# Performance work log

Measured on AMD Instinct MI355X. Metric: run time of the kernel, lower is better.

The kernel has to match this reference:

```python
import jax, jax.numpy as jnp
import numpy as np

NUM_USERS = 100000
NUM_ITEMS = 50000
NUM_EDGES = 4000000
EMB_DIM = 64
K_HOPS = 3


def setup_inputs() -> dict:
    key = jax.random.key(0)
    k1, k2, k3, k4, k5, k6 = jax.random.split(key, 6)
    N = NUM_USERS + NUM_ITEMS
    return {
        "users_emb": jax.random.normal(k1, (NUM_USERS, EMB_DIM), dtype=jnp.float32) * 0.1,
        "items_emb": jax.random.normal(k2, (NUM_ITEMS, EMB_DIM), dtype=jnp.float32) * 0.1,
        "edge_row": jax.random.randint(k3, (NUM_EDGES,), 0, N, dtype=jnp.int32),
        "edge_col": jax.random.randint(k4, (NUM_EDGES,), 0, N, dtype=jnp.int32),
        "user_id": jax.random.randint(k5, (4096,), 0, NUM_USERS, dtype=jnp.int32),
        "item_ids": jax.random.randint(k6, (4096,), 0, NUM_ITEMS, dtype=jnp.int32),
    }


def reference(users_emb, items_emb, edge_row, edge_col, user_id, item_ids):
    num_users = users_emb.shape[0]
    N = num_users + items_emb.shape[0]
    dt = users_emb.dtype

    # gcn_norm (no self loops): deg = rowsum of A, w_e = d_r^{-1/2} d_c^{-1/2}
    deg = jax.ops.segment_sum(jnp.ones(edge_row.shape[0], dtype=dt), edge_row,
                              num_segments=N)
    deg_inv_sqrt = jnp.where(deg > 0, 1.0 / jnp.sqrt(jnp.where(deg > 0, deg, 1.0)), 0.0)
    w = deg_inv_sqrt[edge_row] * deg_inv_sqrt[edge_col]  # [E]

    emb = jnp.concatenate([users_emb, items_emb], axis=0)  # [N, D]
    acc = emb  # running sum of K+1 layer snapshots
    for _ in range(K_HOPS):
        # SpMM: out[r] += w_e * emb[c]
        emb = jax.ops.segment_sum(w[:, None] * emb[edge_col], edge_row,
                                  num_segments=N)
        acc = acc + emb
    emb_final = acc / (K_HOPS + 1)  # layer-mean pooling

    users_final = emb_final[user_id]               # [B, D]
    items_final = emb_final[num_users + item_ids]  # [B, D]
    return jnp.concatenate([users_final, items_final], axis=1)  # [B, 2D]
```

## Files before the change

kernel.cpp:

```cpp
#include <hip/hip_runtime.h>
#include <hip/hip_bf16.h>

#define NUSERS 100000
#define NITEMS 50000
#define NN (NUSERS + NITEMS)
#define NE 4000000
#define DIM 64
#define BQ 4096
#define NBIN ((NN + 255) >> 8)
#define BINCAP 9216
#define EPB2 8192

typedef unsigned short u16;
typedef unsigned int u32;
typedef float v2f __attribute__((ext_vector_type(2)));
typedef unsigned u32x2 __attribute__((ext_vector_type(2)));

__device__ __forceinline__ float bf2f(u16 u) {
    return __uint_as_float(((unsigned)u) << 16);
}
__device__ __forceinline__ u16 f2bf(float f) {
    unsigned x = __float_as_uint(f);
    return (u16)((x + 0x7FFFu + ((x >> 16) & 1u)) >> 16);
}
__device__ __forceinline__ void add8p(v2f* acc2, uint4 u) {
    acc2[0] += (v2f){__uint_as_float(u.x << 16), __uint_as_float(u.x & 0xffff0000u)};
    acc2[1] += (v2f){__uint_as_float(u.y << 16), __uint_as_float(u.y & 0xffff0000u)};
    acc2[2] += (v2f){__uint_as_float(u.z << 16), __uint_as_float(u.z & 0xffff0000u)};
    acc2[3] += (v2f){__uint_as_float(u.w << 16), __uint_as_float(u.w & 0xffff0000u)};
}
__device__ __forceinline__ uint4 ld_row(const char* __restrict__ base, int c, int dgoff) {
    u32 off = ((u32)c << 7) + (u32)dgoff;
    return *(const uint4*)(base + off);
}

#if __has_builtin(__builtin_amdgcn_update_dpp)
__device__ __forceinline__ float xadd8(float x) {
    int y = __builtin_amdgcn_update_dpp(0, __float_as_int(x), 0x128, 0xF, 0xF, true);
    return x + __int_as_float(y);
}
#else
__device__ __forceinline__ float xadd8(float x) { return x + __shfl_xor(x, 8, 64); }
#endif
#if __has_builtin(__builtin_amdgcn_permlane16_swap)
__device__ __forceinline__ float xadd16(float x) {
    u32x2 r = __builtin_amdgcn_permlane16_swap(__float_as_uint(x), __float_as_uint(x),
                                               false, false);
    return __uint_as_float(r.x) + __uint_as_float(r.y);
}
#else
__device__ __forceinline__ float xadd16(float x) { return x + __shfl_xor(x, 16, 64); }
#endif
#if __has_builtin(__builtin_amdgcn_permlane32_swap)
__device__ __forceinline__ float xadd32(float x) {
    u32x2 r = __builtin_amdgcn_permlane32_swap(__float_as_uint(x), __float_as_uint(x),
                                               false, false);
    return __uint_as_float(r.x) + __uint_as_float(r.y);
}
#else
__device__ __forceinline__ float xadd32(float x) { return x + __shfl_xor(x, 32, 64); }
#endif

__device__ __forceinline__ void reduce_acc(v2f* acc2) {
#pragma unroll
    for (int j = 0; j < 4; ++j) { acc2[j].x = xadd8(acc2[j].x);  acc2[j].y = xadd8(acc2[j].y);  }
#pragma unroll
    for (int j = 0; j < 4; ++j) { acc2[j].x = xadd16(acc2[j].x); acc2[j].y = xadd16(acc2[j].y); }
#pragma unroll
    for (int j = 0; j < 4; ++j) { acc2[j].x = xadd32(acc2[j].x); acc2[j].y = xadd32(acc2[j].y); }
}

template<int G>
__device__ __forceinline__ void rowsum_fix(const int* __restrict__ col_s, int start,
                                           int eslot, const char* __restrict__ inb,
                                           int dgoff, v2f* acc2) {
    int cg[G];
#pragma unroll
    for (int g = 0; g < G; ++g) cg[g] = col_s[start + (g << 3) + eslot];
    uint4 v[G];
#pragma unroll
    for (int g = 0; g < G; ++g) v[g] = ld_row(inb, cg[g], dgoff);
#if __has_builtin(__builtin_amdgcn_sched_barrier)
    __builtin_amdgcn_sched_barrier(0);
#endif
#pragma unroll
    for (int g = 0; g < G; ++g) add8p(acc2, v[g]);
}

__device__ __forceinline__ void rowsum_core(int start, int n8,
                                            const int* __restrict__ col_s,
                                            const char* __restrict__ inb,
                                            int eslot, int dgoff, v2f* acc2) {
    switch (n8 >> 3) {
    case 0: break;
    case 1: rowsum_fix<1>(col_s, start, eslot, inb, dgoff, acc2); break;
    case 2: rowsum_fix<2>(col_s, start, eslot, inb, dgoff, acc2); break;
    case 3: rowsum_fix<3>(col_s, start, eslot, inb, dgoff, acc2); break;
    case 4: rowsum_fix<4>(col_s, start, eslot, inb, dgoff, acc2); break;
    case 5: rowsum_fix<5>(col_s, start, eslot, inb, dgoff, acc2); break;
    case 6: rowsum_fix<6>(col_s, start, eslot, inb, dgoff, acc2); break;
    case 7: rowsum_fix<7>(col_s, start, eslot, inb, dgoff, acc2); break;
    case 8: rowsum_fix<8>(col_s, start, eslot, inb, dgoff, acc2); break;
    default: {
        int i = eslot;
        int c0 = col_s[start + i];
        uint4 v0 = ld_row(inb, c0, dgoff);
        for (i += 8; i < n8; i += 8) {
            int c1 = col_s[start + i];
            uint4 v1 = ld_row(inb, c1, dgoff);
            add8p(acc2, v0);
            v0 = v1;
        }
        add8p(acc2, v0);
    }
    }
}

__global__ void k_init(int* __restrict__ bin_cur, u32* __restrict__ m2w,
                       u16* __restrict__ ea, u16* __restrict__ eb) {
    int t = blockIdx.x * blockDim.x + threadIdx.x;
    if (t < NBIN) bin_cur[t] = t * BINCAP;
    if (t < 37504) m2w[t] = 0;
    if (t < 32) {
        ((u32*)(ea + (size_t)NN * DIM))[t] = 0;
        ((u32*)(eb + (size_t)NN * DIM))[t] = 0;
    }
}

__global__ void __launch_bounds__(1024) k_binA2(
        const int* __restrict__ row, const int* __restrict__ col,
        int* __restrict__ bin_cur, u32* __restrict__ pairs, int E) {
    __shared__ u32 stage[EPB2];
    __shared__ int hist[NBIN];
    __shared__ int base_l[NBIN];
    __shared__ int cbase[NBIN];
    __shared__ int lcur[NBIN];
    __shared__ int s[1024];
    int t = threadIdx.x;
    int base = blockIdx.x * EPB2;
    int lim = min(E - base, EPB2);

    if (t < NBIN) hist[t] = 0;
    __syncthreads();

    for (int i = t; i < lim; i += 1024)
        atomicAdd(&hist[row[base + i] >> 8], 1);
    __syncthreads();

    int v = (t < NBIN) ? hist[t] : 0;
    s[t] = v;
    __syncthreads();
    for (int off = 1; off < 1024; off <<= 1) {
        int x = (t >= off) ? s[t - off] : 0;
        __syncthreads();
        s[t] += x;
        __syncthreads();
    }
    if (t < NBIN) {
        int excl = s[t] - v;
        base_l[t] = excl;
        lcur[t] = excl;
        cbase[t] = (v > 0) ? atomicAdd(&bin_cur[t], v) : 0;
    }
    __syncthreads();

    for (int i = t; i < lim; i += 1024) {
        int r = row[base + i];
        int c = col[base + i];
        int pos = atomicAdd(&lcur[r >> 8], 1);
        stage[pos] = ((u32)(r & 255) << 24) | (u32)c;
    }
    __syncthreads();

    int wv = t >> 6;
    int lane = t & 63;
    for (int b = wv; b < NBIN; b += 16) {
        int h = hist[b];
        int lb = base_l[b];
        size_t gb = (size_t)cbase[b];
        for (int i = lane; i < h; i += 64)
            pairs[gb + i] = stage[lb + i];
    }
}

__global__ void __launch_bounds__(1024) k_binB(
        const u32* __restrict__ pairs, const int* __restrict__ bin_cur,
        int* __restrict__ col_s, int* __restrict__ rs, int* __restrict__ deg) {
    __shared__ int cnt[256];
    __shared__ int pscan[256];
    __shared__ int cur[256];
    int b = blockIdx.x;
    int t = threadIdx.x;
    int base = b * BINCAP;
    int end = bin_cur[b];
    if (t < 256) cnt[t] = 0;
    __syncthreads();
    for (int i = base + t; i < end; i += 1024)
        atomicAdd(&cnt[pairs[i] >> 24], 1);
    __syncthreads();
    int v = (t < 256) ? cnt[t] : 0;
    int pv = (v + 7) & ~7;
    if (t < 256) pscan[t] = pv;
    __syncthreads();
    for (int off = 1; off < 256; off <<= 1) {
        int x = (t >= off && t < 256) ? pscan[t - off] : 0;
        __syncthreads();
        if (t < 256) pscan[t] += x;
        __syncthreads();
    }
    if (t < 256) {
        int rowstart = base + pscan[t] - pv;
        int r = (b << 8) + t;
        if (r < NN) {
            rs[r] = rowstart;
            deg[r] = v;
        }
        cur[t] = rowstart;
        for (int i = v; i < pv; ++i) col_s[rowstart + i] = NN;
    }
    __syncthreads();
    for (int i = base + t; i < end; i += 1024) {
        u32 p = pairs[i];
        int pos = atomicAdd(&cur[p >> 24], 1);
        col_s[pos] = (int)(p & 0x00FFFFFFu);
    }
}

__global__ void k_concat_t0(const float* __restrict__ u, const float* __restrict__ it,
                            const int* __restrict__ deg, u16* __restrict__ emb) {
    int i = blockIdx.x * blockDim.x + threadIdx.x;
    const int NU4 = NUSERS * DIM / 4;
    const int NT4 = NN * DIM / 4;
    if (i >= NT4) return;
    int row = i >> 4;
    int d = deg[row];
    float sc = (d > 0) ? (1.0f / sqrtf((float)d)) : 0.0f;
    float4 v = (i < NU4) ? ((const float4*)u)[i] : ((const float4*)it)[i - NU4];
    ushort4 o;
    o.x = f2bf(sc * v.x); o.y = f2bf(sc * v.y);
    o.z = f2bf(sc * v.z); o.w = f2bf(sc * v.w);
    ((ushort4*)emb)[i] = o;
}

__global__ void k_mark(const int* __restrict__ uid, const int* __restrict__ iid,
                       const int* __restrict__ rs, const int* __restrict__ deg,
                       const int* __restrict__ col_s, unsigned char* __restrict__ m2) {
    int q = (blockIdx.x * blockDim.x + threadIdx.x) >> 6;
    if (q >= 2 * BQ) return;
    int lane = threadIdx.x & 63;
    int r = (q < BQ) ? uid[q] : (NUSERS + iid[q - BQ]);
    if (lane == 0) m2[r] = 1;
    int s = rs[r], n = deg[r];
    for (int i = lane; i < n; i += 64) m2[col_s[s + i]] = 1;
}

__global__ void __launch_bounds__(256) k_spmm8(
        const int* __restrict__ rs, const int* __restrict__ deg,
        const int* __restrict__ col_s, const u16* __restrict__ in,
        u16* __restrict__ out, const unsigned char* __restrict__ mask) {
    int wid = (blockIdx.x * blockDim.x + threadIdx.x) >> 6;
    if (wid >= NN) return;
    if (mask && !mask[wid]) return;
    int lane = threadIdx.x & 63;
    int eslot = lane >> 3;
    int dg = lane & 7;
    int dgoff = dg << 4;
    int n = deg[wid];
    int start = rs[wid];
    int n8 = (n + 7) & ~7;
    const char* inb = (const char*)in;
    v2f acc2[4] = {(v2f)0.f, (v2f)0.f, (v2f)0.f, (v2f)0.f};
    if (n8 > 0)
        rowsum_core(start, n8, col_s, inb, eslot, dgoff, acc2);
    reduce_acc(acc2);
    if (eslot == 0) {
        float s = (n > 0) ? (1.0f / (float)n) : 0.0f;
        v2f vs = {s, s};
        u32 p[4];
#pragma unroll
        for (int j = 0; j < 4; ++j) {
            v2f r = acc2[j] * vs;
            __hip_bfloat162 h = __float22bfloat162_rn(make_float2(r.x, r.y));
            p[j] = *(u32*)&h;
        }
        ((uint4*)out)[(size_t)wid * 8 + dg] = make_uint4(p[0], p[1], p[2], p[3]);
    }
}

__global__ void __launch_bounds__(256) k_spmm_out(
        const int* __restrict__ rs, const int* __restrict__ deg,
        const int* __restrict__ col_s, const u16* __restrict__ in,
        const int* __restrict__ uid, const int* __restrict__ iid,
        float* __restrict__ out) {
    int q = (blockIdx.x * blockDim.x + threadIdx.x) >> 6;
    if (q >= 2 * BQ) return;
    int lane = threadIdx.x & 63;
    int eslot = lane >> 3;
    int dg = lane & 7;
    int dgoff = dg << 4;
    int b, r, off;
    if (q < BQ) { b = q; r = uid[q]; off = 0; }
    else { b = q - BQ; r = NUSERS + iid[q - BQ]; off = DIM; }
    int n = deg[r];
    int start = rs[r];
    int n8 = (n + 7) & ~7;
    const char* inb = (const char*)in;
    v2f acc2[4] = {(v2f)0.f, (v2f)0.f, (v2f)0.f, (v2f)0.f};
    if (n8 > 0)
        rowsum_core(start, n8, col_s, inb, eslot, dgoff, acc2);
    reduce_acc(acc2);
    if (eslot == 0) {
        float dr = (n > 0) ? (1.0f / sqrtf((float)n)) : 0.0f;
        float* o = out + (size_t)b * (2 * DIM) + off + dg * 8;
#pragma unroll
        for (int j = 0; j < 4; ++j) {
            o[2 * j]     = (o[2 * j]     + dr * acc2[j].x) * 0.25f;
            o[2 * j + 1] = (o[2 * j + 1] + dr * acc2[j].y) * 0.25f;
        }
    }
}


__global__ void k_gather_init(const int* __restrict__ uid, const int* __restrict__ iid,
                              const float* __restrict__ u, const float* __restrict__ it,
                              float* __restrict__ out) {
    int t = blockIdx.x * blockDim.x + threadIdx.x;
    if (t >= BQ * DIM) return;
    int b = t >> 6;
    int d = t & 63;
    out[b * (2 * DIM) + d]       = u[(size_t)uid[b] * DIM + d];
    out[b * (2 * DIM) + DIM + d] = it[(size_t)iid[b] * DIM + d];
}

__global__ void k_gather_add(const int* __restrict__ uid, const int* __restrict__ iid,
                             const int* __restrict__ deg, const u16* __restrict__ emb,
                             float* __restrict__ out) {
    int t = blockIdx.x * blockDim.x + threadIdx.x;
    if (t >= BQ * DIM) return;
    int b = t >> 6;
    int d = t & 63;
    int ru = uid[b];
    int ri = NUSERS + iid[b];
    int du = deg[ru], di = deg[ri];
    float su = (du > 0) ? sqrtf((float)du) : 0.0f;
    float si = (di > 0) ? sqrtf((float)di) : 0.0f;
    int ou = b * (2 * DIM) + d;
    int oi = ou + DIM;
    out[ou] = out[ou] + su * bf2f(emb[(size_t)ru * DIM + d]);
    out[oi] = out[oi] + si * bf2f(emb[(size_t)ri * DIM + d]);
}


extern "C" void kernel_launch(void* const* d_in, const int* in_sizes, int n_in,
                              void* d_out, int out_size, void* d_ws, size_t ws_size,
                              hipStream_t stream) {
    const float* users_emb = (const float*)d_in[0];
    const float* items_emb = (const float*)d_in[1];
    const int*   edge_row  = (const int*)d_in[2];
    const int*   edge_col  = (const int*)d_in[3];
    const int*   user_id   = (const int*)d_in[4];
    const int*   item_ids  = (const int*)d_in[5];
    float* out = (float*)d_out;

    char* ws = (char*)d_ws;
    int*   deg_i   = (int*)  (ws + 0);
    int*   rs      = (int*)  (ws + 655360);
    int*   bin_cur = (int*)  (ws + 1310720);
    unsigned char* m2 = (unsigned char*)(ws + 1400000);
    int*   col_s   = (int*)  (ws + 4194304);
    u32*   pairs   = (u32*)  (ws + 29360128);
    u16*   emb_a   = (u16*)  (ws + 54525952);
    u16*   emb_b   = (u16*)  (ws + 75497472);

    k_init<<<147, 256, 0, stream>>>(bin_cur, (u32*)m2, emb_a, emb_b);

    k_binA2<<<(NE + EPB2 - 1) / EPB2, 1024, 0, stream>>>(edge_row, edge_col, bin_cur,
                                                         pairs, NE);
    k_binB<<<NBIN, 1024, 0, stream>>>(pairs, bin_cur, col_s, rs, deg_i);

    k_concat_t0<<<(NN * DIM / 4 + 255) / 256, 256, 0, stream>>>(users_emb, items_emb,
                                                                deg_i, emb_a);

    k_gather_init<<<(BQ * DIM + 255) / 256, 256, 0, stream>>>(user_id, item_ids,
                                                              users_emb, items_emb, out);

    k_mark<<<(2 * BQ + 3) / 4, 256, 0, stream>>>(user_id, item_ids, rs, deg_i, col_s, m2);

    const int spmm_blocks = (NN + 3) / 4;
    k_spmm8<<<spmm_blocks, 256, 0, stream>>>(rs, deg_i, col_s, emb_a, emb_b,
                                             (const unsigned char*)nullptr);
    k_gather_add<<<(BQ * DIM + 255) / 256, 256, 0, stream>>>(user_id, item_ids, deg_i,
                                                             emb_b, out);
    k_spmm8<<<spmm_blocks, 256, 0, stream>>>(rs, deg_i, col_s, emb_b, emb_a, m2);
    k_gather_add<<<(BQ * DIM + 255) / 256, 256, 0, stream>>>(user_id, item_ids, deg_i,
                                                             emb_a, out);
    k_spmm_out<<<(2 * BQ + 3) / 4, 256, 0, stream>>>(rs, deg_i, col_s, emb_a,
                                                     user_id, item_ids, out);
}
```

Before: 307.7 us.

## Replace per-row SpMM with persistent software-pipelined kernel using packed row metadata

Replaces the one-wave-per-row SpMM with a persistent grid of 1024 blocks in which each wave strides over rows. The loop is software-pipelined: metadata for row i+3 is loaded, column indices for row i+2 are fetched, and embedding gathers for row i+1 are issued while row i is reduced and stored. Row start and degree are packed into an int2 array written by the binning kernel, so each row needs one metadata load. The aim is to hide gather latency and remove per-row launch and scheduling overhead, at the cost of many more live registers and lower occupancy; the masked pass also reads mask bytes for rows it will skip.

```diff
diff --git a/kernel.cpp b/kernel.cpp
--- a/kernel.cpp
+++ b/kernel.cpp
@@ -68,6 +68,113 @@
     for (int j = 0; j < 4; ++j) { acc2[j].x = xadd16(acc2[j].x); acc2[j].y = xadd16(acc2[j].y); }
 #pragma unroll
     for (int j = 0; j < 4; ++j) { acc2[j].x = xadd32(acc2[j].x); acc2[j].y = xadd32(acc2[j].y); }
+}
+
+struct MetaS { int s; int n; int m; };
+
+template<bool MASKED>
+__device__ __forceinline__ MetaS ldmeta(const int2* __restrict__ meta2,
+                                        const unsigned char* __restrict__ mask, int r) {
+    MetaS t; t.s = 0; t.n = 0; t.m = 0;
+    if (r < NN) {
+        int2 v = meta2[r];
+        t.s = v.x; t.n = v.y;
+        t.m = MASKED ? (int)mask[r] : 1;
+    }
+    return t;
+}
+
+__device__ __forceinline__ void ldcols(int* cg, const int* __restrict__ col_s,
+                                       MetaS mt, int eslot) {
+    int n8 = (mt.n + 7) & ~7;
+    int lim = mt.m ? n8 : 0;
+#pragma unroll
+    for (int g = 0; g < 8; ++g) {
+        int c = col_s[mt.s + (g << 3) + eslot];
+        cg[g] = ((g << 3) < lim) ? c : NN;
+    }
+}
+
+__device__ __forceinline__ void issue4(uint4* v, const char* __restrict__ base2,
+                                       const int* cg, int lo) {
+#pragma unroll
+    for (int g = 0; g < 4; ++g)
+        v[g] = *(const uint4*)(base2 + (((u32)cg[lo + g]) << 7));
+}
+
+__device__ __forceinline__ void consume_store(const uint4* v, int big, MetaS mt,
+        const int* __restrict__ col_s, const char* __restrict__ base2,
+        int eslot, int dg, u16* __restrict__ out, int r) {
+    v2f acc2[4] = {(v2f)0.f, (v2f)0.f, (v2f)0.f, (v2f)0.f};
+#pragma unroll
+    for (int g = 0; g < 4; ++g) add8p(acc2, v[g]);
+    if (big) {
+#pragma unroll
+        for (int g = 4; g < 8; ++g) add8p(acc2, v[g]);
+    }
+    int n8 = (mt.n + 7) & ~7;
+    if (n8 > 64) {
+        for (int i = 64 + eslot; i < n8; i += 8) {
+            int c = col_s[mt.s + i];
+            uint4 u = *(const uint4*)(base2 + (((u32)c) << 7));
+            add8p(acc2, u);
+        }
+    }
+    reduce_acc(acc2);
+    if (eslot == 0) {
+        float sc = (mt.n > 0) ? (1.0f / (float)mt.n) : 0.0f;
+        v2f vs = {sc, sc};
+        u32 p[4];
+#pragma unroll
+        for (int j = 0; j < 4; ++j) {
+            v2f t = acc2[j] * vs;
+            __hip_bfloat162 h = __float22bfloat162_rn(make_float2(t.x, t.y));
+            p[j] = *(u32*)&h;
+        }
+        ((uint4*)out)[(size_t)r * 8 + dg] = make_uint4(p[0], p[1], p[2], p[3]);
+    }
+}
+
+template<bool MASKED>
+__global__ void __launch_bounds__(256) k_spmm_p(
+        const int2* __restrict__ meta2, const int* __restrict__ col_s,
+        const u16* __restrict__ in, u16* __restrict__ out,
+        const unsigned char* __restrict__ mask) {
+    int lane = threadIdx.x & 63;
+    int eslot = lane >> 3, dg = lane & 7;
+    const char* base2 = (const char*)in + (dg << 4);
+    const int nw = gridDim.x << 2;
+    int r = ((blockIdx.x << 8) + threadIdx.x) >> 6;
+
+    MetaS M0 = ldmeta<MASKED>(meta2, mask, r);
+    MetaS M1 = ldmeta<MASKED>(meta2, mask, r + nw);
+    MetaS M2 = ldmeta<MASKED>(meta2, mask, r + 2 * nw);
+    int cgA[8], cgB[8];
+    uint4 vA[8], vB[8];
+    ldcols(cgA, col_s, M0, eslot);
+    int bigA = M0.m & (M0.n > 32), bigB = 0;
+    if (M0.m)  issue4(vA, base2, cgA, 0);
+    if (bigA)  issue4(vA + 4, base2, cgA, 4);
+    ldcols(cgB, col_s, M1, eslot);
+
+    for (;;) {
+        bigB = M1.m & (M1.n > 32);
+        if (M1.m) issue4(vB, base2, cgB, 0);
+        if (bigB) issue4(vB + 4, base2, cgB, 4);
+        ldcols(cgA, col_s, M2, eslot);
+        MetaS M3 = ldmeta<MASKED>(meta2, mask, r + 3 * nw);
+        if (M0.m) consume_store(vA, bigA, M0, col_s, base2, eslot, dg, out, r);
+        r += nw; if (r >= NN) break;
+        M0 = M1; M1 = M2; M2 = M3;
+        bigA = M1.m & (M1.n > 32);
+        if (M1.m) issue4(vA, base2, cgA, 0);
+        if (bigA) issue4(vA + 4, base2, cgA, 4);
+        ldcols(cgB, col_s, M2, eslot);
+        M3 = ldmeta<MASKED>(meta2, mask, r + 3 * nw);
+        if (M0.m) consume_store(vB, bigB, M0, col_s, base2, eslot, dg, out, r);
+        r += nw; if (r >= NN) break;
+        M0 = M1; M1 = M2; M2 = M3;
+    }
 }
 
 template<int G>
@@ -185,7 +292,8 @@
 
 __global__ void __launch_bounds__(1024) k_binB(
         const u32* __restrict__ pairs, const int* __restrict__ bin_cur,
-        int* __restrict__ col_s, int* __restrict__ rs, int* __restrict__ deg) {
+        int* __restrict__ col_s, int* __restrict__ rs, int* __restrict__ deg,
+        int2* __restrict__ meta2) {
     __shared__ int cnt[256];
     __shared__ int pscan[256];
     __shared__ int cur[256];
@@ -214,6 +322,7 @@
         if (r < NN) {
             rs[r] = rowstart;
             deg[r] = v;
+            meta2[r] = make_int2(rowstart, v);
         }
         cur[t] = rowstart;
         for (int i = v; i < pv; ++i) col_s[rowstart + i] = NN;
@@ -252,39 +361,6 @@
     if (lane == 0) m2[r] = 1;
     int s = rs[r], n = deg[r];
     for (int i = lane; i < n; i += 64) m2[col_s[s + i]] = 1;
-}
-
-__global__ void __launch_bounds__(256) k_spmm8(
-        const int* __restrict__ rs, const int* __restrict__ deg,
-        const int* __restrict__ col_s, const u16* __restrict__ in,
-        u16* __restrict__ out, const unsigned char* __restrict__ mask) {
-    int wid = (blockIdx.x * blockDim.x + threadIdx.x) >> 6;
-    if (wid >= NN) return;
-    if (mask && !mask[wid]) return;
-    int lane = threadIdx.x & 63;
-    int eslot = lane >> 3;
-    int dg = lane & 7;
-    int dgoff = dg << 4;
-    int n = deg[wid];
-    int start = rs[wid];
-    int n8 = (n + 7) & ~7;
-    const char* inb = (const char*)in;
-    v2f acc2[4] = {(v2f)0.f, (v2f)0.f, (v2f)0.f, (v2f)0.f};
-    if (n8 > 0)
-        rowsum_core(start, n8, col_s, inb, eslot, dgoff, acc2);
-    reduce_acc(acc2);
-    if (eslot == 0) {
-        float s = (n > 0) ? (1.0f / (float)n) : 0.0f;
-        v2f vs = {s, s};
-        u32 p[4];
-#pragma unroll
-        for (int j = 0; j < 4; ++j) {
-            v2f r = acc2[j] * vs;
-            __hip_bfloat162 h = __float22bfloat162_rn(make_float2(r.x, r.y));
-            p[j] = *(u32*)&h;
-        }
-        ((uint4*)out)[(size_t)wid * 8 + dg] = make_uint4(p[0], p[1], p[2], p[3]);
-    }
 }
 
 __global__ void __launch_bounds__(256) k_spmm_out(
@@ -367,6 +443,7 @@
     int*   rs      = (int*)  (ws + 655360);
     int*   bin_cur = (int*)  (ws + 1310720);
     unsigned char* m2 = (unsigned char*)(ws + 1400000);
+    int2*  meta2   = (int2*) (ws + 2097152);
     int*   col_s   = (int*)  (ws + 4194304);
     u32*   pairs   = (u32*)  (ws + 29360128);
     u16*   emb_a   = (u16*)  (ws + 54525952);
@@ -376,7 +453,7 @@
 
     k_binA2<<<(NE + EPB2 - 1) / EPB2, 1024, 0, stream>>>(edge_row, edge_col, bin_cur,
                                                          pairs, NE);
-    k_binB<<<NBIN, 1024, 0, stream>>>(pairs, bin_cur, col_s, rs, deg_i);
+    k_binB<<<NBIN, 1024, 0, stream>>>(pairs, bin_cur, col_s, rs, deg_i, meta2);
 
     k_concat_t0<<<(NN * DIM / 4 + 255) / 256, 256, 0, stream>>>(users_emb, items_emb,
                                                                 deg_i, emb_a);
@@ -386,12 +463,11 @@
 
     k_mark<<<(2 * BQ + 3) / 4, 256, 0, stream>>>(user_id, item_ids, rs, deg_i, col_s, m2);
 
-    const int spmm_blocks = (NN + 3) / 4;
-    k_spmm8<<<spmm_blocks, 256, 0, stream>>>(rs, deg_i, col_s, emb_a, emb_b,
-                                             (const unsigned char*)nullptr);
+    k_spmm_p<false><<<1024, 256, 0, stream>>>(meta2, col_s, emb_a, emb_b,
+                                              (const unsigned char*)nullptr);
     k_gather_add<<<(BQ * DIM + 255) / 256, 256, 0, stream>>>(user_id, item_ids, deg_i,
                                                              emb_b, out);
-    k_spmm8<<<spmm_blocks, 256, 0, stream>>>(rs, deg_i, col_s, emb_b, emb_a, m2);
+    k_spmm_p<true><<<1024, 256, 0, stream>>>(meta2, col_s, emb_b, emb_a, m2);
     k_gather_add<<<(BQ * DIM + 255) / 256, 256, 0, stream>>>(user_id, item_ids, deg_i,
                                                              emb_a, out);
     k_spmm_out<<<(2 * BQ + 3) / 4, 256, 0, stream>>>(rs, deg_i, col_s, emb_a,
```

New measurement: 341.9 us. 1.11x slower.

## Process two rows per wavefront in SpMM with packed row metadata

Applied to the files above, without the earlier changes.

Rewrites the SpMM kernels so each 64-lane wavefront handles two rows, 32 lanes each with 4 edge slots. The earlier design used one wave per row with 8 edge slots. Row start and degree are packed into one int2 array written by the binning kernel, so a single load replaces two. Edge loops become fixed batches of 8 loads with a wave-uniform tail loop instead of a degree switch. The aim is to cut idle lanes and reduction steps for the low average degree (~27), at the cost of divergence when paired rows have different degrees.

```diff
diff --git a/kernel.cpp b/kernel.cpp
--- a/kernel.cpp
+++ b/kernel.cpp
@@ -29,10 +29,6 @@
     acc2[2] += (v2f){__uint_as_float(u.z << 16), __uint_as_float(u.z & 0xffff0000u)};
     acc2[3] += (v2f){__uint_as_float(u.w << 16), __uint_as_float(u.w & 0xffff0000u)};
 }
-__device__ __forceinline__ uint4 ld_row(const char* __restrict__ base, int c, int dgoff) {
-    u32 off = ((u32)c << 7) + (u32)dgoff;
-    return *(const uint4*)(base + off);
-}
 
 #if __has_builtin(__builtin_amdgcn_update_dpp)
 __device__ __forceinline__ float xadd8(float x) {
@@ -51,68 +47,122 @@
 #else
 __device__ __forceinline__ float xadd16(float x) { return x + __shfl_xor(x, 16, 64); }
 #endif
-#if __has_builtin(__builtin_amdgcn_permlane32_swap)
-__device__ __forceinline__ float xadd32(float x) {
-    u32x2 r = __builtin_amdgcn_permlane32_swap(__float_as_uint(x), __float_as_uint(x),
-                                               false, false);
-    return __uint_as_float(r.x) + __uint_as_float(r.y);
-}
+
+#if __has_builtin(__builtin_amdgcn_sched_barrier)
+#define SCHED_FENCE() __builtin_amdgcn_sched_barrier(0)
 #else
-__device__ __forceinline__ float xadd32(float x) { return x + __shfl_xor(x, 32, 64); }
+#define SCHED_FENCE()
 #endif
 
-__device__ __forceinline__ void reduce_acc(v2f* acc2) {
+__device__ __forceinline__ void reduce_half(v2f* acc2) {
 #pragma unroll
     for (int j = 0; j < 4; ++j) { acc2[j].x = xadd8(acc2[j].x);  acc2[j].y = xadd8(acc2[j].y);  }
 #pragma unroll
     for (int j = 0; j < 4; ++j) { acc2[j].x = xadd16(acc2[j].x); acc2[j].y = xadd16(acc2[j].y); }
-#pragma unroll
-    for (int j = 0; j < 4; ++j) { acc2[j].x = xadd32(acc2[j].x); acc2[j].y = xadd32(acc2[j].y); }
-}
-
-template<int G>
-__device__ __forceinline__ void rowsum_fix(const int* __restrict__ col_s, int start,
-                                           int eslot, const char* __restrict__ inb,
-                                           int dgoff, v2f* acc2) {
-    int cg[G];
-#pragma unroll
-    for (int g = 0; g < G; ++g) cg[g] = col_s[start + (g << 3) + eslot];
-    uint4 v[G];
-#pragma unroll
-    for (int g = 0; g < G; ++g) v[g] = ld_row(inb, cg[g], dgoff);
-#if __has_builtin(__builtin_amdgcn_sched_barrier)
-    __builtin_amdgcn_sched_barrier(0);
-#endif
-#pragma unroll
-    for (int g = 0; g < G; ++g) add8p(acc2, v[g]);
-}
-
-__device__ __forceinline__ void rowsum_core(int start, int n8,
-                                            const int* __restrict__ col_s,
-                                            const char* __restrict__ inb,
-                                            int eslot, int dgoff, v2f* acc2) {
-    switch (n8 >> 3) {
-    case 0: break;
-    case 1: rowsum_fix<1>(col_s, start, eslot, inb, dgoff, acc2); break;
-    case 2: rowsum_fix<2>(col_s, start, eslot, inb, dgoff, acc2); break;
-    case 3: rowsum_fix<3>(col_s, start, eslot, inb, dgoff, acc2); break;
-    case 4: rowsum_fix<4>(col_s, start, eslot, inb, dgoff, acc2); break;
-    case 5: rowsum_fix<5>(col_s, start, eslot, inb, dgoff, acc2); break;
-    case 6: rowsum_fix<6>(col_s, start, eslot, inb, dgoff, acc2); break;
-    case 7: rowsum_fix<7>(col_s, start, eslot, inb, dgoff, acc2); break;
-    case 8: rowsum_fix<8>(col_s, start, eslot, inb, dgoff, acc2); break;
-    default: {
-        int i = eslot;
-        int c0 = col_s[start + i];
-        uint4 v0 = ld_row(inb, c0, dgoff);
-        for (i += 8; i < n8; i += 8) {
-            int c1 = col_s[start + i];
-            uint4 v1 = ld_row(inb, c1, dgoff);
-            add8p(acc2, v0);
-            v0 = v1;
-        }
-        add8p(acc2, v0);
-    }
+}
+
+__device__ __forceinline__ void batch8(const int* __restrict__ col_s, int start,
+                                       int s0, int lim, int eslot,
+                                       const char* __restrict__ base2, v2f* acc2) {
+    int cg[8];
+#pragma unroll
+    for (int g = 0; g < 8; ++g) {
+        int slot = s0 + (g << 2) + eslot;
+        int c = col_s[start + slot];
+        cg[g] = (slot < lim) ? c : NN;
+    }
+    uint4 v[8];
+#pragma unroll
+    for (int g = 0; g < 8; ++g)
+        v[g] = *(const uint4*)(base2 + (((u32)cg[g]) << 7));
+    SCHED_FENCE();
+#pragma unroll
+    for (int g = 0; g < 8; ++g) add8p(acc2, v[g]);
+}
+
+template<bool MASKED>
+__global__ void __launch_bounds__(256) k_spmm2(
+        const int2* __restrict__ meta2, const int* __restrict__ col_s,
+        const u16* __restrict__ in, u16* __restrict__ out,
+        const unsigned char* __restrict__ mask) {
+    int wid = (blockIdx.x * blockDim.x + threadIdx.x) >> 6;
+    int lane = threadIdx.x & 63;
+    int half = lane >> 5;
+    int eslot = (lane >> 3) & 3;
+    int dg = lane & 7;
+    int r = (wid << 1) + half;
+    int2 mv = meta2[r];
+    int start = mv.x, n = mv.y;
+    int m = MASKED ? (int)mask[r] : 1;
+    int n8 = (n + 7) & ~7;
+    int lim = m ? n8 : 0;
+    if (MASKED && !__any(lim > 0)) return;
+    const char* base2 = (const char*)in + (dg << 4);
+
+    v2f acc2[4] = {(v2f)0.f, (v2f)0.f, (v2f)0.f, (v2f)0.f};
+    batch8(col_s, start, 0, lim, eslot, base2, acc2);
+    if (__any(lim > 32))
+        batch8(col_s, start, 32, lim, eslot, base2, acc2);
+    if (__any(lim > 64)) {
+        for (int i = 64 + eslot; i < lim; i += 4) {
+            int c = col_s[start + i];
+            uint4 u = *(const uint4*)(base2 + (((u32)c) << 7));
+            add8p(acc2, u);
+        }
+    }
+    reduce_half(acc2);
+    if (eslot == 0 && m) {
+        float sc = (n > 0) ? (1.0f / (float)n) : 0.0f;
+        v2f vs = {sc, sc};
+        u32 p[4];
+#pragma unroll
+        for (int j = 0; j < 4; ++j) {
+            v2f t = acc2[j] * vs;
+            __hip_bfloat162 h = __float22bfloat162_rn(make_float2(t.x, t.y));
+            p[j] = *(u32*)&h;
+        }
+        ((uint4*)out)[(size_t)r * 8 + dg] = make_uint4(p[0], p[1], p[2], p[3]);
+    }
+}
+
+__global__ void __launch_bounds__(256) k_spmm_out2(
+        const int2* __restrict__ meta2, const int* __restrict__ col_s,
+        const u16* __restrict__ in, const int* __restrict__ uid,
+        const int* __restrict__ iid, float* __restrict__ out) {
+    int wid = (blockIdx.x * blockDim.x + threadIdx.x) >> 6;
+    int lane = threadIdx.x & 63;
+    int half = lane >> 5;
+    int eslot = (lane >> 3) & 3;
+    int dg = lane & 7;
+    int q = (wid << 1) + half;
+    int b, r, off;
+    if (q < BQ) { b = q; r = uid[q]; off = 0; }
+    else { b = q - BQ; r = NUSERS + iid[q - BQ]; off = DIM; }
+    int2 mv = meta2[r];
+    int start = mv.x, n = mv.y;
+    int n8 = (n + 7) & ~7;
+    const char* base2 = (const char*)in + (dg << 4);
+
+    v2f acc2[4] = {(v2f)0.f, (v2f)0.f, (v2f)0.f, (v2f)0.f};
+    batch8(col_s, start, 0, n8, eslot, base2, acc2);
+    if (__any(n8 > 32))
+        batch8(col_s, start, 32, n8, eslot, base2, acc2);
+    if (__any(n8 > 64)) {
+        for (int i = 64 + eslot; i < n8; i += 4) {
+            int c = col_s[start + i];
+            uint4 u = *(const uint4*)(base2 + (((u32)c) << 7));
+            add8p(acc2, u);
+        }
+    }
+    reduce_half(acc2);
+    if (eslot == 0) {
+        float dr = (n > 0) ? (1.0f / sqrtf((float)n)) : 0.0f;
+        float* o = out + (size_t)b * (2 * DIM) + off + dg * 8;
+#pragma unroll
+        for (int j = 0; j < 4; ++j) {
+            o[2 * j]     = (o[2 * j]     + dr * acc2[j].x) * 0.25f;
+            o[2 * j + 1] = (o[2 * j + 1] + dr * acc2[j].y) * 0.25f;
+        }
     }
 }
 
@@ -185,7 +235,8 @@
 
 __global__ void __launch_bounds__(1024) k_binB(
         const u32* __restrict__ pairs, const int* __restrict__ bin_cur,
-        int* __restrict__ col_s, int* __restrict__ rs, int* __restrict__ deg) {
+        int* __restrict__ col_s, int* __restrict__ rs, int* __restrict__ deg,
+        int2* __restrict__ meta2) {
     __shared__ int cnt[256];
     __shared__ int pscan[256];
     __shared__ int cur[256];
@@ -214,6 +265,7 @@
         if (r < NN) {
             rs[r] = rowstart;
             deg[r] = v;
+            meta2[r] = make_int2(rowstart, v);
         }
         cur[t] = rowstart;
         for (int i = v; i < pv; ++i) col_s[rowstart + i] = NN;
@@ -252,72 +304,6 @@
     if (lane == 0) m2[r] = 1;
     int s = rs[r], n = deg[r];
     for (int i = lane; i < n; i += 64) m2[col_s[s + i]] = 1;
-}
-
-__global__ void __launch_bounds__(256) k_spmm8(
-        const int* __restrict__ rs, const int* __restrict__ deg,
-        const int* __restrict__ col_s, const u16* __restrict__ in,
-        u16* __restrict__ out, const unsigned char* __restrict__ mask) {
-    int wid = (blockIdx.x * blockDim.x + threadIdx.x) >> 6;
-    if (wid >= NN) return;
-    if (mask && !mask[wid]) return;
-    int lane = threadIdx.x & 63;
-    int eslot = lane >> 3;
-    int dg = lane & 7;
-    int dgoff = dg << 4;
-    int n = deg[wid];
-    int start = rs[wid];
-    int n8 = (n + 7) & ~7;
-    const char* inb = (const char*)in;
-    v2f acc2[4] = {(v2f)0.f, (v2f)0.f, (v2f)0.f, (v2f)0.f};
-    if (n8 > 0)
-        rowsum_core(start, n8, col_s, inb, eslot, dgoff, acc2);
-    reduce_acc(acc2);
-    if (eslot == 0) {
-        float s = (n > 0) ? (1.0f / (float)n) : 0.0f;
-        v2f vs = {s, s};
-        u32 p[4];
-#pragma unroll
-        for (int j = 0; j < 4; ++j) {
-            v2f r = acc2[j] * vs;
-            __hip_bfloat162 h = __float22bfloat162_rn(make_float2(r.x, r.y));
-            p[j] = *(u32*)&h;
-        }
-        ((uint4*)out)[(size_t)wid * 8 + dg] = make_uint4(p[0], p[1], p[2], p[3]);
-    }
-}
-
-__global__ void __launch_bounds__(256) k_spmm_out(
-        const int* __restrict__ rs, const int* __restrict__ deg,
-        const int* __restrict__ col_s, const u16* __restrict__ in,
-        const int* __restrict__ uid, const int* __restrict__ iid,
-        float* __restrict__ out) {
-    int q = (blockIdx.x * blockDim.x + threadIdx.x) >> 6;
-    if (q >= 2 * BQ) return;
-    int lane = threadIdx.x & 63;
-    int eslot = lane >> 3;
-    int dg = lane & 7;
-    int dgoff = dg << 4;
-    int b, r, off;
-    if (q < BQ) { b = q; r = uid[q]; off = 0; }
-    else { b = q - BQ; r = NUSERS + iid[q - BQ]; off = DIM; }
-    int n = deg[r];
-    int start = rs[r];
-    int n8 = (n + 7) & ~7;
-    const char* inb = (const char*)in;
-    v2f acc2[4] = {(v2f)0.f, (v2f)0.f, (v2f)0.f, (v2f)0.f};
-    if (n8 > 0)
-        rowsum_core(start, n8, col_s, inb, eslot, dgoff, acc2);
-    reduce_acc(acc2);
-    if (eslot == 0) {
-        float dr = (n > 0) ? (1.0f / sqrtf((float)n)) : 0.0f;
-        float* o = out + (size_t)b * (2 * DIM) + off + dg * 8;
-#pragma unroll
-        for (int j = 0; j < 4; ++j) {
-            o[2 * j]     = (o[2 * j]     + dr * acc2[j].x) * 0.25f;
-            o[2 * j + 1] = (o[2 * j + 1] + dr * acc2[j].y) * 0.25f;
-        }
-    }
 }
 
 
@@ -367,6 +353,7 @@
     int*   rs      = (int*)  (ws + 655360);
     int*   bin_cur = (int*)  (ws + 1310720);
     unsigned char* m2 = (unsigned char*)(ws + 1400000);
+    int2*  meta2   = (int2*) (ws + 2097152);
     int*   col_s   = (int*)  (ws + 4194304);
     u32*   pairs   = (u32*)  (ws + 29360128);
     u16*   emb_a   = (u16*)  (ws + 54525952);
@@ -376,7 +363,7 @@
 
     k_binA2<<<(NE + EPB2 - 1) / EPB2, 1024, 0, stream>>>(edge_row, edge_col, bin_cur,
                                                          pairs, NE);
-    k_binB<<<NBIN, 1024, 0, stream>>>(pairs, bin_cur, col_s, rs, deg_i);
+    k_binB<<<NBIN, 1024, 0, stream>>>(pairs, bin_cur, col_s, rs, deg_i, meta2);
 
     k_concat_t0<<<(NN * DIM / 4 + 255) / 256, 256, 0, stream>>>(users_emb, items_emb,
                                                                 deg_i, emb_a);
@@ -386,14 +373,12 @@
 
     k_mark<<<(2 * BQ + 3) / 4, 256, 0, stream>>>(user_id, item_ids, rs, deg_i, col_s, m2);
 
-    const int spmm_blocks = (NN + 3) / 4;
-    k_spmm8<<<spmm_blocks, 256, 0, stream>>>(rs, deg_i, col_s, emb_a, emb_b,
-                                             (const unsigned char*)nullptr);
+    k_spmm2<false><<<18750, 256, 0, stream>>>(meta2, col_s, emb_a, emb_b,
+                                              (const unsigned char*)nullptr);
     k_gather_add<<<(BQ * DIM + 255) / 256, 256, 0, stream>>>(user_id, item_ids, deg_i,
                                                              emb_b, out);
-    k_spmm8<<<spmm_blocks, 256, 0, stream>>>(rs, deg_i, col_s, emb_b, emb_a, m2);
+    k_spmm2<true><<<18750, 256, 0, stream>>>(meta2, col_s, emb_b, emb_a, m2);
     k_gather_add<<<(BQ * DIM + 255) / 256, 256, 0, stream>>>(user_id, item_ids, deg_i,
                                                              emb_a, out);
-    k_spmm_out<<<(2 * BQ + 3) / 4, 256, 0, stream>>>(rs, deg_i, col_s, emb_a,
-                                                     user_id, item_ids, out);
-}
+    k_spmm_out2<<<1024, 256, 0, stream>>>(meta2, col_s, emb_a, user_id, item_ids, out);
+}
```

After: 296.3 us. 1.04x faster.
